# Kernel tuning notes

Measured on AMD Instinct MI355X. Metric: run time of the kernel, lower is better.

Reference implementation:

```python
import jax, jax.numpy as jnp
import numpy as np

B, C, S, H, W = 8, 64, 64, 128, 128
HID = 32           # max(C//2, 8)
STEPS, DT, OMEGA_MAX = 10, 0.3, 2.0
EPS = 1e-5


def _dw(x, k):
    # depthwise 3x3 conv, NCHW, kernel [C,1,3,3]
    return jax.lax.conv_general_dilated(
        x, k, (1, 1), 'SAME',
        dimension_numbers=('NCHW', 'OIHW', 'NCHW'),
        feature_group_count=x.shape[1])


def _pw(x, w, b=None):
    # pointwise (1x1) conv as einsum, w: [out,in]
    y = jnp.einsum('bihw,oi->bohw', x, w)
    return y if b is None else y + b[None, :, None, None]


def _lrelu(x):
    return jax.nn.leaky_relu(x, 0.2)


def setup_inputs() -> dict:
    key = jax.random.key(0)
    ks = jax.random.split(key, 16)
    d = {
        'force': jax.random.normal(ks[0], (B, C, H, W), jnp.float32),
        'style': jax.random.normal(ks[1], (1, S, 1, 1), jnp.float32),
        'illum_feat': jax.random.normal(ks[2], (B, C, H, W), jnp.float32),
        # HyperEncoder 1x1 convs
        'h_w1': 0.05 * jax.random.normal(ks[3], (HID, C + S), jnp.float32),
        'h_b1': jnp.zeros((HID,), jnp.float32),
        'h_w2': 0.05 * jax.random.normal(ks[4], (HID, HID), jnp.float32),
        'h_b2': jnp.zeros((HID,), jnp.float32),
        'h_w3': 0.05 * jax.random.normal(ks[5], (4 * C, HID), jnp.float32),
        'h_b3': jnp.zeros((4 * C,), jnp.float32),
        # OscillatorCell convs (no bias)
        'dw_k': 0.05 * jax.random.normal(ks[6], (C, 1, 3, 3), jnp.float32),
        'pw_w': 0.05 * jax.random.normal(ks[7], (C, C), jnp.float32),
        # refine: dw3x3 (+bias), pw, lrelu, pw
        'r_dw_k': 0.05 * jax.random.normal(ks[8], (C, 1, 3, 3), jnp.float32),
        'r_dw_b': jnp.zeros((C,), jnp.float32),
        'r_pw1_w': 0.05 * jax.random.normal(ks[9], (C, C), jnp.float32),
        'r_pw1_b': jnp.zeros((C,), jnp.float32),
        'r_pw2_w': 0.05 * jax.random.normal(ks[10], (C, C), jnp.float32),
        'r_pw2_b': jnp.zeros((C,), jnp.float32),
        'layer_scale': 0.01 * jnp.ones((1, C, 1, 1), jnp.float32),
    }
    return d


def reference(force, style, illum_feat,
              h_w1, h_b1, h_w2, h_b2, h_w3, h_b3,
              dw_k, pw_w,
              r_dw_k, r_dw_b, r_pw1_w, r_pw1_b, r_pw2_w, r_pw2_b,
              layer_scale):
    force = force + 0.2 * illum_feat
    b, c, h, w = force.shape

    # HyperEncoder
    style_map = jnp.broadcast_to(style, (b, style.shape[1], h, w))
    u = jnp.concatenate([force, style_map], axis=1)
    u = _lrelu(_pw(u, h_w1, h_b1))
    u = _lrelu(_pw(u, h_w2, h_b2))
    p = _pw(u, h_w3, h_b3)
    wch, zch, gch, bch = jnp.split(p, 4, axis=1)
    omega = jax.nn.sigmoid(wch) * OMEGA_MAX
    zeta = jax.nn.sigmoid(zch)
    gamma = jax.nn.sigmoid(gch) * 2.0
    beta = jnp.tanh(bch)

    # unrolled symplectic-Euler oscillator recurrence
    def step(carry, _):
        x, v = carry
        coupling = _dw(x, dw_k) + _pw(x, pw_w)
        accel = force + coupling - 2.0 * zeta * omega * v - omega ** 2 * x
        v = v + accel * DT
        x = x + v * DT
        return (x, v), None

    x0 = jnp.zeros_like(force)
    (x, v), _ = jax.lax.scan(step, (x0, x0), None, length=STEPS)

    # instance norm (no affine) + style modulation
    fx = force + x
    mu = fx.mean(axis=(2, 3), keepdims=True)
    var = fx.var(axis=(2, 3), keepdims=True)
    out = gamma * ((fx - mu) / jnp.sqrt(var + EPS)) + beta

    # refine branch with layer scale
    r = _dw(out, r_dw_k) + r_dw_b[None, :, None, None]
    r = _lrelu(_pw(r, r_pw1_w, r_pw1_b))
    r = _pw(r, r_pw2_w, r_pw2_b)
    out = out + layer_scale * r
    return (out, x, v)
```

## Files before the change

### kernel.cpp

```cpp
#include <hip/hip_runtime.h>
#include <hip/hip_fp16.h>

#define Hn 128
#define Wn 128
#define HWn 16384
#define Cn 64
#define Bn 8
#define NTOT (Bn*Cn*HWn)
#define NPIX (Bn*HWn)
#define DTc 0.3f
#define EPSc 1e-5f

__device__ __forceinline__ float sigm(float t){ return 1.0f/(1.0f+__expf(-t)); }

__global__ void prep(const float* __restrict__ style, const float* __restrict__ w1,
                     const float* __restrict__ b1, const float* __restrict__ pw,
                     const float* __restrict__ pw1, const float* __restrict__ pw2,
                     const float* __restrict__ w3, const float* __restrict__ b3,
                     float* __restrict__ w1T, float* __restrict__ c1,
                     float* __restrict__ pwT, float* __restrict__ pw1T,
                     float* __restrict__ pw2T,
                     __half2* __restrict__ w3abP, __half2* __restrict__ w3gbP,
                     __half2* __restrict__ b3abP, __half2* __restrict__ b3gbP)
{
    int t = threadIdx.x;
    if (t < 32) {
        float s = b1[t];
        for (int k = 0; k < 64; k++) s += w1[t*128 + 64 + k] * style[k];
        c1[t] = s;
    }
    for (int i = t; i < 2048; i += 256) { int c = i >> 5, j = i & 31; w1T[i] = w1[j*128 + c]; }
    for (int i = t; i < 4096; i += 256) {
        int c = i >> 6, k = i & 63;
        pwT[i]  = pw[k*64 + c];
        pw1T[i] = pw1[k*64 + c];
        pw2T[i] = pw2[k*64 + c];
    }
    for (int i = t; i < 2048; i += 256) {
        int j = i >> 5, k = i & 31;
        w3abP[i] = __floats2half2_rn(w3[j*32 + k],         w3[(64 + j)*32 + k]);
        w3gbP[i] = __floats2half2_rn(w3[(128 + j)*32 + k], w3[(192 + j)*32 + k]);
    }
    if (t < 64) {
        b3abP[t] = __floats2half2_rn(b3[t],       b3[64 + t]);
        b3gbP[t] = __floats2half2_rn(b3[128 + t], b3[192 + t]);
    }
}

__global__ __launch_bounds__(256)
void hyperU(const float4* __restrict__ force4, const float4* __restrict__ illum4,
            const float* __restrict__ w1T, const float* __restrict__ c1,
            const float* __restrict__ w2, const float* __restrict__ b2,
            __half* __restrict__ F, __half* __restrict__ XA, __half* __restrict__ Vh,
            __half* __restrict__ U2)
{
    __shared__ __half fs[64][256];
    int t = threadIdx.x;
    int p0 = blockIdx.x << 8;
    int b  = p0 >> 14;
    int sp0 = p0 & (HWn - 1);
    size_t tbase = (size_t)b * Cn * HWn + sp0;
    size_t tb4   = tbase >> 2;

#pragma unroll
    for (int it = 0; it < 16; it++) {
        int f = t + (it << 8);
        int c = f >> 6, u = f & 63;
        size_t gi = tb4 + (size_t)c * (HWn >> 2) + u;
        float4 fv = force4[gi], iv = illum4[gi];
        __half2 h0 = __floats2half2_rn(fv.x + 0.2f*iv.x, fv.y + 0.2f*iv.y);
        __half2 h1 = __floats2half2_rn(fv.z + 0.2f*iv.z, fv.w + 0.2f*iv.w);
        uint2 pk; pk.x = *(unsigned int*)&h0; pk.y = *(unsigned int*)&h1;
        *reinterpret_cast<uint2*>(&fs[c][u << 2]) = pk;
    }
    __syncthreads();

#pragma unroll
    for (int it = 0; it < 8; it++) {
        int f = t + (it << 8);
        int c = f >> 5, u = f & 31;
        uint4 d = *reinterpret_cast<const uint4*>(&fs[c][u << 3]);
        size_t gi = tbase + (size_t)c * HWn + (u << 3);
        *reinterpret_cast<uint4*>(F + gi) = d;
        uint4 xk, vk;
        unsigned int* dp = &d.x;
        unsigned int* xp = &xk.x;
        unsigned int* vp = &vk.x;
#pragma unroll
        for (int q = 0; q < 4; q++) {
            float2 fv = __half22float2(*(__half2*)&dp[q]);
            __half2 hx = __floats2half2_rn(0.09f*fv.x, 0.09f*fv.y);
            __half2 hv = __floats2half2_rn(0.3f*fv.x,  0.3f*fv.y);
            xp[q] = *(unsigned int*)&hx;
            vp[q] = *(unsigned int*)&hv;
        }
        *reinterpret_cast<uint4*>(XA + gi) = xk;
        *reinterpret_cast<uint4*>(Vh + gi) = vk;
    }

    float u1[32];
#pragma unroll
    for (int j = 0; j < 32; j++) u1[j] = c1[j];
#pragma unroll 4
    for (int c = 0; c < 64; c++) {
        float fc = __half2float(fs[c][t]);
        const float* __restrict__ wr = w1T + c*32;
#pragma unroll
        for (int j = 0; j < 32; j++) u1[j] += wr[j] * fc;
    }
#pragma unroll
    for (int j = 0; j < 32; j++) { float v = u1[j]; u1[j] = v > 0.f ? v : 0.2f*v; }

    float u2[32];
#pragma unroll
    for (int i = 0; i < 32; i++) {
        float s = b2[i];
#pragma unroll
        for (int j = 0; j < 32; j++) s += w2[i*32 + j] * u1[j];
        u2[i] = s > 0.f ? s : 0.2f*s;
    }

    uint4* dst = reinterpret_cast<uint4*>(U2 + ((size_t)(p0 + t)) * 32);
#pragma unroll
    for (int q = 0; q < 4; q++) {
        __half2 h0 = __floats2half2_rn(u2[8*q+0], u2[8*q+1]);
        __half2 h1 = __floats2half2_rn(u2[8*q+2], u2[8*q+3]);
        __half2 h2 = __floats2half2_rn(u2[8*q+4], u2[8*q+5]);
        __half2 h3 = __floats2half2_rn(u2[8*q+6], u2[8*q+7]);
        uint4 d;
        d.x = *(unsigned int*)&h0; d.y = *(unsigned int*)&h1;
        d.z = *(unsigned int*)&h2; d.w = *(unsigned int*)&h3;
        dst[q] = d;
    }
}

__global__ __launch_bounds__(256)
void hyperA(const __half* __restrict__ U2,
            const __half2* __restrict__ w3abP, const __half2* __restrict__ b3abP,
            __half2* __restrict__ AB)
{
    int p = blockIdx.x * blockDim.x + threadIdx.x;
    int j0 = blockIdx.y << 5;
    int b  = p >> 14;
    int sp = p & (HWn - 1);
    int base = b * Cn * HWn + sp;

    __half2 u2b[32];
    const uint4* src = reinterpret_cast<const uint4*>(U2 + (size_t)p * 32);
#pragma unroll
    for (int q = 0; q < 4; q++) {
        uint4 d = src[q];
        __half2 h;
        h = *(__half2*)&d.x; u2b[8*q+0] = __half2half2(__low2half(h)); u2b[8*q+1] = __half2half2(__high2half(h));
        h = *(__half2*)&d.y; u2b[8*q+2] = __half2half2(__low2half(h)); u2b[8*q+3] = __half2half2(__high2half(h));
        h = *(__half2*)&d.z; u2b[8*q+4] = __half2half2(__low2half(h)); u2b[8*q+5] = __half2half2(__high2half(h));
        h = *(__half2*)&d.w; u2b[8*q+6] = __half2half2(__low2half(h)); u2b[8*q+7] = __half2half2(__high2half(h));
    }

#pragma unroll 2
    for (int jj = 0; jj < 32; jj++) {
        int j = j0 + jj;
        __half2 aab = b3abP[j];
        const __half2* __restrict__ wa = w3abP + j*32;
#pragma unroll
        for (int i = 0; i < 32; i++) aab = __hfma2(wa[i], u2b[i], aab);
        float2 tab = __half22float2(aab);
        float om = 2.0f * sigm(tab.x);
        float ze = sigm(tab.y);
        AB[base + j*HWn] = __floats2half2_rn(2.0f * ze * om, om * om);
    }
}

template <bool LAST>
__global__ void osc_step(const __half* __restrict__ Xin, __half* __restrict__ Xout,
                         __half* __restrict__ V, const __half* __restrict__ F,
                         const __half2* __restrict__ AB,
                         const float* __restrict__ dwk, const float* __restrict__ pwT,
                         float* __restrict__ Xf, float* __restrict__ Vf)
{
    int wid  = blockIdx.x;
    int slot = wid >> 3;
    int pc   = ((wid & 7) << 6) + (slot >> 2);
    int c0   = (slot & 3) << 4;
    int p = (pc << 8) + threadIdx.x;
    int b  = p >> 14;
    int sp = p & (HWn - 1);
    int y = sp >> 7, x = sp & 127;
    int base = b * Cn * HWn + sp;

    float acc[16];
#pragma unroll
    for (int k = 0; k < 16; k++) acc[k] = 0.f;
#pragma unroll 4
    for (int c = 0; c < 64; c++) {
        float xc = __half2float(Xin[base + c*HWn]);
        const float* __restrict__ wr = pwT + c*64 + c0;
#pragma unroll
        for (int k = 0; k < 16; k++) acc[k] += wr[k] * xc;
    }

    int   yo[3] = { y > 0 ? -Wn : 0, 0, y < Hn-1 ? Wn : 0 };
    int   xo[3] = { x > 0 ? -1  : 0, 0, x < Wn-1 ? 1  : 0 };
    float my[3] = { y > 0 ? 1.f : 0.f, 1.f, y < Hn-1 ? 1.f : 0.f };
    float mx[3] = { x > 0 ? 1.f : 0.f, 1.f, x < Wn-1 ? 1.f : 0.f };
    float mm[9]; int oo[9];
#pragma unroll
    for (int dy = 0; dy < 3; dy++)
#pragma unroll
        for (int dx = 0; dx < 3; dx++) { mm[dy*3+dx] = my[dy]*mx[dx]; oo[dy*3+dx] = yo[dy]+xo[dx]; }

#pragma unroll
    for (int cc = 0; cc < 16; cc++) {
        int c = c0 + cc;
        int cb = base + c*HWn;
        float tv[9];
#pragma unroll
        for (int t = 0; t < 9; t++) tv[t] = __half2float(Xin[cb + oo[t]]);
        float dws = 0.f;
#pragma unroll
        for (int t = 0; t < 9; t++) dws += (dwk[c*9 + t] * mm[t]) * tv[t];
        float xc = tv[4];
        float2 ab = __half22float2(AB[cb]);
        float vv = __half2float(V[cb]);
        float accel = __half2float(F[cb]) + acc[cc] + dws - ab.x * vv - ab.y * xc;
        vv += accel * DTc;
        float xn = xc + vv * DTc;
        if constexpr (!LAST) {
            V[cb] = __float2half(vv);
            Xout[cb] = __float2half(xn);
        } else {
            Xf[cb] = xn;
            Vf[cb] = vv;
        }
    }
}

__global__ void inorm_stats(const __half* __restrict__ F, const float* __restrict__ X,
                            float* __restrict__ mu, float* __restrict__ rs)
{
    int bc = blockIdx.x;
    int base = bc * HWn;
    const __half2* __restrict__ F2 = (const __half2*)(F + base);
    const float4*  __restrict__ X4 = (const float4*)(X + base);
    float s = 0.f, s2 = 0.f;
    for (int i = threadIdx.x; i < HWn/4; i += blockDim.x) {
        float4 xv = X4[i];
        float2 f0 = __half22float2(F2[2*i]);
        float2 f1 = __half22float2(F2[2*i+1]);
        float v0 = f0.x + xv.x, v1 = f0.y + xv.y, v2 = f1.x + xv.z, v3 = f1.y + xv.w;
        s += (v0 + v1) + (v2 + v3);
        s2 += (v0*v0 + v1*v1) + (v2*v2 + v3*v3);
    }
#pragma unroll
    for (int o = 32; o > 0; o >>= 1) { s += __shfl_down(s, o); s2 += __shfl_down(s2, o); }
    __shared__ float sh[16];
    int w = threadIdx.x >> 6, l = threadIdx.x & 63;
    if (l == 0) { sh[w] = s; sh[8 + w] = s2; }
    __syncthreads();
    if (threadIdx.x == 0) {
        float S = 0.f, S2 = 0.f;
        for (int i = 0; i < 4; i++) { S += sh[i]; S2 += sh[8 + i]; }
        float m = S / (float)HWn;
        float var = S2 / (float)HWn - m*m;
        mu[bc] = m;
        rs[bc] = rsqrtf(var + EPSc);
    }
}

__global__ __launch_bounds__(256)
void modGB(const __half* __restrict__ U2, const __half* __restrict__ F,
           const float* __restrict__ X,
           const __half2* __restrict__ w3gbP, const __half2* __restrict__ b3gbP,
           const float* __restrict__ mu, const float* __restrict__ rs,
           __half* __restrict__ outp)
{
    int p = blockIdx.x * blockDim.x + threadIdx.x;
    int j0 = blockIdx.y << 4;
    int b  = p >> 14;
    int sp = p & (HWn - 1);
    int base = b * Cn * HWn + sp;

    __half2 u2b[32];
    const uint4* src = reinterpret_cast<const uint4*>(U2 + (size_t)p * 32);
#pragma unroll
    for (int q = 0; q < 4; q++) {
        uint4 d = src[q];
        __half2 h;
        h = *(__half2*)&d.x; u2b[8*q+0] = __half2half2(__low2half(h)); u2b[8*q+1] = __half2half2(__high2half(h));
        h = *(__half2*)&d.y; u2b[8*q+2] = __half2half2(__low2half(h)); u2b[8*q+3] = __half2half2(__high2half(h));
        h = *(__half2*)&d.z; u2b[8*q+4] = __half2half2(__low2half(h)); u2b[8*q+5] = __half2half2(__high2half(h));
        h = *(__half2*)&d.w; u2b[8*q+6] = __half2half2(__low2half(h)); u2b[8*q+7] = __half2half2(__high2half(h));
    }

#pragma unroll 2
    for (int jj = 0; jj < 16; jj++) {
        int j = j0 + jj;
        __half2 agb = b3gbP[j];
        const __half2* __restrict__ wg = w3gbP + j*32;
#pragma unroll
        for (int i = 0; i < 32; i++) agb = __hfma2(wg[i], u2b[i], agb);
        float2 tgb = __half22float2(agb);
        float gamma = 2.0f * sigm(tgb.x);
        float beta  = tanhf(tgb.y);
        int cb = base + j*HWn;
        int bc = b*64 + j;
        float fx = __half2float(F[cb]) + X[cb];
        float o = gamma * ((fx - mu[bc]) * rs[bc]) + beta;
        outp[cb] = __float2half(o);
    }
}

__global__ __launch_bounds__(512)
void refine(const __half* __restrict__ outp,
            const float* __restrict__ rdwk, const float* __restrict__ rdwb,
            const float* __restrict__ pw1T, const float* __restrict__ pb1,
            const float* __restrict__ pw2T, const float* __restrict__ pb2,
            const float* __restrict__ ls, float* __restrict__ out)
{
    __shared__ unsigned int rv2_s[64][64];
    __shared__ unsigned int act2_s[64][64];
    __shared__ __half w1s[64][64];
    __shared__ __half w2s[64][64];
    __shared__ float  dwks[576];
    __shared__ __half2 pb1h[32], pb2h[32];
    __shared__ float  rdwbs[64], lss[64];
    int t = threadIdx.x;
    for (int i = t; i < 4096; i += 512) {
        w1s[i>>6][i&63] = __float2half(pw1T[i]);
        w2s[i>>6][i&63] = __float2half(pw2T[i]);
    }
    for (int i = t; i < 576; i += 512) dwks[i] = rdwk[i];
    if (t < 64) { rdwbs[t]=rdwb[t]; lss[t]=ls[t]; }
    if (t < 32) {
        pb1h[t] = __floats2half2_rn(pb1[2*t], pb1[2*t+1]);
        pb2h[t] = __floats2half2_rn(pb2[2*t], pb2[2*t+1]);
    }

    int l  = t & 63;
    int g  = t >> 6;
    int c0 = g << 3;
    int row = blockIdx.x;
    int b = row >> 7, y = row & 127;
    int base = b * Cn * HWn + y * Wn;
    int px0 = l << 1;

    int   yo[3] = { y > 0 ? -Wn : 0, 0, y < Hn-1 ? Wn : 0 };
    float my[3] = { y > 0 ? 1.f : 0.f, 1.f, y < Hn-1 ? 1.f : 0.f };
    float wl = l > 0  ? 1.f : 0.f;
    float wr = l < 63 ? 1.f : 0.f;
    int loff = l > 0 ? -1 : 0;
    __syncthreads();

#pragma unroll
    for (int cc = 0; cc < 8; cc++) {
        int c = c0 + cc;
        int cb = base + c*HWn + px0;
        float rv0 = rdwbs[c], rv1 = rdwbs[c];
#pragma unroll
        for (int r = 0; r < 3; r++) {
            const __half* __restrict__ rp = outp + cb + yo[r];
            unsigned int cu = *reinterpret_cast<const unsigned int*>(rp);
            float2 ct = __half22float2(*(__half2*)&cu);
            float lf = __half2float(rp[loff]);
            float rt = __half2float(rp[2]);
            float k0 = dwks[c*9 + r*3 + 0] * my[r];
            float k1 = dwks[c*9 + r*3 + 1] * my[r];
            float k2 = dwks[c*9 + r*3 + 2] * my[r];
            rv0 += k0*(wl*lf) + k1*ct.x + k2*ct.y;
            rv1 += k0*ct.x + k1*ct.y + k2*(wr*rt);
        }
        __half2 hv = __floats2half2_rn(rv0, rv1);
        rv2_s[c][l] = *(unsigned int*)&hv;
    }
    __syncthreads();

    __half2 accA[4], accB[4];
#pragma unroll
    for (int q = 0; q < 4; q++) { accA[q] = pb1h[(c0 >> 1) + q]; accB[q] = accA[q]; }
#pragma unroll 8
    for (int c = 0; c < 64; c++) {
        unsigned int rvu = rv2_s[c][l];
        __half2 rvp = *(__half2*)&rvu;
        __half2 r0 = __half2half2(__low2half(rvp));
        __half2 r1 = __half2half2(__high2half(rvp));
        uint4 wq = *reinterpret_cast<const uint4*>(&w1s[c][c0]);
        __half2 w01 = *(__half2*)&wq.x, w23 = *(__half2*)&wq.y;
        __half2 w45 = *(__half2*)&wq.z, w67 = *(__half2*)&wq.w;
        accA[0] = __hfma2(w01, r0, accA[0]); accB[0] = __hfma2(w01, r1, accB[0]);
        accA[1] = __hfma2(w23, r0, accA[1]); accB[1] = __hfma2(w23, r1, accB[1]);
        accA[2] = __hfma2(w45, r0, accA[2]); accB[2] = __hfma2(w45, r1, accB[2]);
        accA[3] = __hfma2(w67, r0, accA[3]); accB[3] = __hfma2(w67, r1, accB[3]);
    }
#pragma unroll
    for (int q = 0; q < 4; q++) {
        float2 a0 = __half22float2(accA[q]);
        float2 a1 = __half22float2(accB[q]);
        float e0 = a0.x > 0.f ? a0.x : 0.2f*a0.x;
        float e1 = a0.y > 0.f ? a0.y : 0.2f*a0.y;
        float e2 = a1.x > 0.f ? a1.x : 0.2f*a1.x;
        float e3 = a1.y > 0.f ? a1.y : 0.2f*a1.y;
        __half2 p0 = __floats2half2_rn(e0, e2);
        __half2 p1 = __floats2half2_rn(e1, e3);
        act2_s[c0 + 2*q][l]     = *(unsigned int*)&p0;
        act2_s[c0 + 2*q + 1][l] = *(unsigned int*)&p1;
    }
    __syncthreads();

#pragma unroll
    for (int q = 0; q < 4; q++) { accA[q] = pb2h[(c0 >> 1) + q]; accB[q] = accA[q]; }
#pragma unroll 8
    for (int j = 0; j < 64; j++) {
        unsigned int au = act2_s[j][l];
        __half2 ap = *(__half2*)&au;
        __half2 a0 = __half2half2(__low2half(ap));
        __half2 a1 = __half2half2(__high2half(ap));
        uint4 wq = *reinterpret_cast<const uint4*>(&w2s[j][c0]);
        __half2 w01 = *(__half2*)&wq.x, w23 = *(__half2*)&wq.y;
        __half2 w45 = *(__half2*)&wq.z, w67 = *(__half2*)&wq.w;
        accA[0] = __hfma2(w01, a0, accA[0]); accB[0] = __hfma2(w01, a1, accB[0]);
        accA[1] = __hfma2(w23, a0, accA[1]); accB[1] = __hfma2(w23, a1, accB[1]);
        accA[2] = __hfma2(w45, a0, accA[2]); accB[2] = __hfma2(w45, a1, accB[2]);
        accA[3] = __hfma2(w67, a0, accA[3]); accB[3] = __hfma2(w67, a1, accB[3]);
    }
#pragma unroll
    for (int q = 0; q < 4; q++) {
        float2 a0 = __half22float2(accA[q]);
        float2 a1 = __half22float2(accB[q]);
        int ca = c0 + 2*q, cb2 = ca + 1;
        int ba = base + ca*HWn + px0;
        int bb = base + cb2*HWn + px0;
        unsigned int oua = *reinterpret_cast<const unsigned int*>(outp + ba);
        unsigned int oub = *reinterpret_cast<const unsigned int*>(outp + bb);
        float2 oa = __half22float2(*(__half2*)&oua);
        float2 ob = __half22float2(*(__half2*)&oub);
        float la = lss[ca], lb = lss[cb2];
        *reinterpret_cast<float2*>(out + ba) = make_float2(oa.x + la*a0.x, oa.y + la*a1.x);
        *reinterpret_cast<float2*>(out + bb) = make_float2(ob.x + lb*a0.y, ob.y + lb*a1.y);
    }
}

extern "C" void kernel_launch(void* const* d_in, const int* in_sizes, int n_in,
                              void* d_out, int out_size, void* d_ws, size_t ws_size,
                              hipStream_t stream)
{
    (void)in_sizes; (void)n_in; (void)out_size; (void)ws_size;
    const float* force   = (const float*)d_in[0];
    const float* style   = (const float*)d_in[1];
    const float* illum   = (const float*)d_in[2];
    const float* h_w1    = (const float*)d_in[3];
    const float* h_b1    = (const float*)d_in[4];
    const float* h_w2    = (const float*)d_in[5];
    const float* h_b2    = (const float*)d_in[6];
    const float* h_w3    = (const float*)d_in[7];
    const float* h_b3    = (const float*)d_in[8];
    const float* dw_k    = (const float*)d_in[9];
    const float* pw_w    = (const float*)d_in[10];
    const float* r_dw_k  = (const float*)d_in[11];
    const float* r_dw_b  = (const float*)d_in[12];
    const float* r_pw1_w = (const float*)d_in[13];
    const float* r_pw1_b = (const float*)d_in[14];
    const float* r_pw2_w = (const float*)d_in[15];
    const float* r_pw2_b = (const float*)d_in[16];
    const float* lscale  = (const float*)d_in[17];

    float* out  = (float*)d_out;
    float* Xf32 = out + (size_t)NTOT;
    float* Vf32 = out + 2*(size_t)NTOT;

    char* w = (char*)d_ws;
    __half2* AB = (__half2*)w; w += (size_t)NTOT*4;
    __half*  F  = (__half*)w;  w += (size_t)NTOT*2;
    __half*  XA = (__half*)w;  w += (size_t)NTOT*2;
    __half*  XB = (__half*)w;  w += (size_t)NTOT*2;
    __half*  Vh = (__half*)w;  w += (size_t)NTOT*2;
    __half*  U2h = (__half*)w; w += (size_t)NPIX*32*2;
    float* w1T  = (float*)w;
    float* c1   = w1T + 2048;
    float* pwT  = c1 + 32;
    float* pw1T = pwT + 4096;
    float* pw2T = pw1T + 4096;
    float* mu   = pw2T + 4096;
    float* rs   = mu + 512;
    __half2* w3abP = (__half2*)(rs + 512);
    __half2* w3gbP = w3abP + 2048;
    __half2* b3abP = w3gbP + 2048;
    __half2* b3gbP = b3abP + 64;
    __half* outp = (__half*)AB;

    prep<<<1, 256, 0, stream>>>(style, h_w1, h_b1, pw_w, r_pw1_w, r_pw2_w, h_w3, h_b3,
                                w1T, c1, pwT, pw1T, pw2T, w3abP, w3gbP, b3abP, b3gbP);
    hyperU<<<NPIX/256, 256, 0, stream>>>((const float4*)force, (const float4*)illum,
                                         w1T, c1, h_w2, h_b2, F, XA, Vh, U2h);
    hyperA<<<dim3(NPIX/256, 2), 256, 0, stream>>>(U2h, w3abP, b3abP, AB);
    for (int s = 1; s <= 8; s++) {
        const __half* xin = (s & 1) ? XA : XB;
        __half*      xout = (s & 1) ? XB : XA;
        osc_step<false><<<2048, 256, 0, stream>>>(xin, xout, Vh, F, AB,
                                                  dw_k, pwT, nullptr, nullptr);
    }
    osc_step<true><<<2048, 256, 0, stream>>>(XA, XB, Vh, F, AB,
                                             dw_k, pwT, Xf32, Vf32);
    inorm_stats<<<Bn*Cn, 256, 0, stream>>>(F, Xf32, mu, rs);
    modGB<<<dim3(NPIX/256, 4), 256, 0, stream>>>(U2h, F, Xf32, w3gbP, b3gbP,
                                                 mu, rs, outp);
    refine<<<NPIX/128, 512, 0, stream>>>(outp, r_dw_k, r_dw_b, pw1T, r_pw1_b,
                                         pw2T, r_pw2_b, lscale, out);
}
```

Baseline: 453.6 us.

## Fuse instance-norm statistics into last oscillator step via atomics

The final oscillator step now reduces sum and sum-of-squares of force+x per block with wavefront shuffles and shared memory, then accumulates per (batch,channel) into global buffers with atomicAdd. A tiny finalize kernel computes the mean and rsqrt of the variance from these sums, replacing a full re-read of X and F by the separate stats kernel. The prep kernel zeroes the accumulators. It also raises the unroll of the pointwise channel loop and hoists the F/V/AB loads ahead of the stencil loads. Atomics make the accumulation order nondeterministic, and the __syncthreads sits inside the unrolled channel loop.

```diff
diff --git a/kernel.cpp b/kernel.cpp
--- a/kernel.cpp
+++ b/kernel.cpp
@@ -21,7 +21,8 @@
                      float* __restrict__ pwT, float* __restrict__ pw1T,
                      float* __restrict__ pw2T,
                      __half2* __restrict__ w3abP, __half2* __restrict__ w3gbP,
-                     __half2* __restrict__ b3abP, __half2* __restrict__ b3gbP)
+                     __half2* __restrict__ b3abP, __half2* __restrict__ b3gbP,
+                     float* __restrict__ Gsum, float* __restrict__ Gsq)
 {
     int t = threadIdx.x;
     if (t < 32) {
@@ -45,6 +46,7 @@
         b3abP[t] = __floats2half2_rn(b3[t],       b3[64 + t]);
         b3gbP[t] = __floats2half2_rn(b3[128 + t], b3[192 + t]);
     }
+    for (int i = t; i < 512; i += 256) { Gsum[i] = 0.f; Gsq[i] = 0.f; }
 }
 
 __global__ __launch_bounds__(256)
@@ -176,13 +178,15 @@
                          __half* __restrict__ V, const __half* __restrict__ F,
                          const __half2* __restrict__ AB,
                          const float* __restrict__ dwk, const float* __restrict__ pwT,
-                         float* __restrict__ Xf, float* __restrict__ Vf)
+                         float* __restrict__ Xf, float* __restrict__ Vf,
+                         float* __restrict__ Gsum, float* __restrict__ Gsq)
 {
     int wid  = blockIdx.x;
     int slot = wid >> 3;
     int pc   = ((wid & 7) << 6) + (slot >> 2);
     int c0   = (slot & 3) << 4;
-    int p = (pc << 8) + threadIdx.x;
+    int t = threadIdx.x;
+    int p = (pc << 8) + t;
     int b  = p >> 14;
     int sp = p & (HWn - 1);
     int y = sp >> 7, x = sp & 127;
@@ -191,7 +195,7 @@
     float acc[16];
 #pragma unroll
     for (int k = 0; k < 16; k++) acc[k] = 0.f;
-#pragma unroll 4
+#pragma unroll 8
     for (int c = 0; c < 64; c++) {
         float xc = __half2float(Xin[base + c*HWn]);
         const float* __restrict__ wr = pwT + c*64 + c0;
@@ -213,16 +217,17 @@
     for (int cc = 0; cc < 16; cc++) {
         int c = c0 + cc;
         int cb = base + c*HWn;
-        float tv[9];
-#pragma unroll
-        for (int t = 0; t < 9; t++) tv[t] = __half2float(Xin[cb + oo[t]]);
-        float dws = 0.f;
-#pragma unroll
-        for (int t = 0; t < 9; t++) dws += (dwk[c*9 + t] * mm[t]) * tv[t];
-        float xc = tv[4];
         float2 ab = __half22float2(AB[cb]);
         float vv = __half2float(V[cb]);
-        float accel = __half2float(F[cb]) + acc[cc] + dws - ab.x * vv - ab.y * xc;
+        float ff = __half2float(F[cb]);
+        float tv[9];
+#pragma unroll
+        for (int tt = 0; tt < 9; tt++) tv[tt] = __half2float(Xin[cb + oo[tt]]);
+        float dws = 0.f;
+#pragma unroll
+        for (int tt = 0; tt < 9; tt++) dws += (dwk[c*9 + tt] * mm[tt]) * tv[tt];
+        float xc = tv[4];
+        float accel = ff + acc[cc] + dws - ab.x * vv - ab.y * xc;
         vv += accel * DTc;
         float xn = xc + vv * DTc;
         if constexpr (!LAST) {
@@ -231,40 +236,34 @@
         } else {
             Xf[cb] = xn;
             Vf[cb] = vv;
+            __shared__ float ssum[16][4], ssq[16][4];
+            float fx = ff + xn;
+            float s = fx, q = fx*fx;
+#pragma unroll
+            for (int o = 32; o > 0; o >>= 1) { s += __shfl_down(s, o); q += __shfl_down(q, o); }
+            int lane = t & 63, wv = t >> 6;
+            if (lane == 0) { ssum[cc][wv] = s; ssq[cc][wv] = q; }
+            if (cc == 15) {
+                __syncthreads();
+                if (t < 16) {
+                    float S = ssum[t][0] + ssum[t][1] + ssum[t][2] + ssum[t][3];
+                    float Q = ssq[t][0]  + ssq[t][1]  + ssq[t][2]  + ssq[t][3];
+                    atomicAdd(&Gsum[b*64 + c0 + t], S);
+                    atomicAdd(&Gsq[b*64 + c0 + t], Q);
+                }
+            }
         }
     }
 }
 
-__global__ void inorm_stats(const __half* __restrict__ F, const float* __restrict__ X,
-                            float* __restrict__ mu, float* __restrict__ rs)
-{
-    int bc = blockIdx.x;
-    int base = bc * HWn;
-    const __half2* __restrict__ F2 = (const __half2*)(F + base);
-    const float4*  __restrict__ X4 = (const float4*)(X + base);
-    float s = 0.f, s2 = 0.f;
-    for (int i = threadIdx.x; i < HWn/4; i += blockDim.x) {
-        float4 xv = X4[i];
-        float2 f0 = __half22float2(F2[2*i]);
-        float2 f1 = __half22float2(F2[2*i+1]);
-        float v0 = f0.x + xv.x, v1 = f0.y + xv.y, v2 = f1.x + xv.z, v3 = f1.y + xv.w;
-        s += (v0 + v1) + (v2 + v3);
-        s2 += (v0*v0 + v1*v1) + (v2*v2 + v3*v3);
-    }
-#pragma unroll
-    for (int o = 32; o > 0; o >>= 1) { s += __shfl_down(s, o); s2 += __shfl_down(s2, o); }
-    __shared__ float sh[16];
-    int w = threadIdx.x >> 6, l = threadIdx.x & 63;
-    if (l == 0) { sh[w] = s; sh[8 + w] = s2; }
-    __syncthreads();
-    if (threadIdx.x == 0) {
-        float S = 0.f, S2 = 0.f;
-        for (int i = 0; i < 4; i++) { S += sh[i]; S2 += sh[8 + i]; }
-        float m = S / (float)HWn;
-        float var = S2 / (float)HWn - m*m;
-        mu[bc] = m;
-        rs[bc] = rsqrtf(var + EPSc);
-    }
+__global__ void inorm_fin(const float* __restrict__ Gsum, const float* __restrict__ Gsq,
+                          float* __restrict__ mu, float* __restrict__ rs)
+{
+    int i = threadIdx.x + blockIdx.x * blockDim.x;
+    float m = Gsum[i] / (float)HWn;
+    float var = Gsq[i] / (float)HWn - m*m;
+    mu[i] = m;
+    rs[i] = rsqrtf(var + EPSc);
 }
 
 __global__ __launch_bounds__(256)
@@ -485,10 +484,13 @@
     __half2* w3gbP = w3abP + 2048;
     __half2* b3abP = w3gbP + 2048;
     __half2* b3gbP = b3abP + 64;
+    float* Gsum = (float*)(b3gbP + 64);
+    float* Gsq  = Gsum + 512;
     __half* outp = (__half*)AB;
 
     prep<<<1, 256, 0, stream>>>(style, h_w1, h_b1, pw_w, r_pw1_w, r_pw2_w, h_w3, h_b3,
-                                w1T, c1, pwT, pw1T, pw2T, w3abP, w3gbP, b3abP, b3gbP);
+                                w1T, c1, pwT, pw1T, pw2T, w3abP, w3gbP, b3abP, b3gbP,
+                                Gsum, Gsq);
     hyperU<<<NPIX/256, 256, 0, stream>>>((const float4*)force, (const float4*)illum,
                                          w1T, c1, h_w2, h_b2, F, XA, Vh, U2h);
     hyperA<<<dim3(NPIX/256, 2), 256, 0, stream>>>(U2h, w3abP, b3abP, AB);
@@ -496,11 +498,12 @@
         const __half* xin = (s & 1) ? XA : XB;
         __half*      xout = (s & 1) ? XB : XA;
         osc_step<false><<<2048, 256, 0, stream>>>(xin, xout, Vh, F, AB,
-                                                  dw_k, pwT, nullptr, nullptr);
+                                                  dw_k, pwT, nullptr, nullptr,
+                                                  nullptr, nullptr);
     }
     osc_step<true><<<2048, 256, 0, stream>>>(XA, XB, Vh, F, AB,
-                                             dw_k, pwT, Xf32, Vf32);
-    inorm_stats<<<Bn*Cn, 256, 0, stream>>>(F, Xf32, mu, rs);
+                                             dw_k, pwT, Xf32, Vf32, Gsum, Gsq);
+    inorm_fin<<<2, 256, 0, stream>>>(Gsum, Gsq, mu, rs);
     modGB<<<dim3(NPIX/256, 4), 256, 0, stream>>>(U2h, F, Xf32, w3gbP, b3gbP,
                                                  mu, rs, outp);
     refine<<<NPIX/128, 512, 0, stream>>>(outp, r_dw_k, r_dw_b, pw1T, r_pw1_b,
```

New measurement: 439.2 us. -3.2%, faster.
